# Kernel tuning notes

Measured on AMD Instinct MI355X. Metric: run time of the kernel, lower is better.

## Reference

```python
import jax, jax.numpy as jnp
import numpy as np

B, CHUNKS, INS, H, H2, OS = 128, 2, 512, 256, 512, 64


def setup_inputs() -> dict:
    key = jax.random.key(0)
    ks = jax.random.split(key, 12)
    s = 1.0 / np.sqrt(H)  # torch default LSTM/Linear init scale
    x = jax.random.normal(ks[0], (B, CHUNKS, INS), dtype=jnp.float32)
    w_ih = jax.random.uniform(ks[1], (4 * H, 1), jnp.float32, -s, s)
    w_hh = jax.random.uniform(ks[2], (4 * H, H), jnp.float32, -s, s)
    b_ih = jax.random.uniform(ks[3], (4 * H,), jnp.float32, -s, s)
    b_hh = jax.random.uniform(ks[4], (4 * H,), jnp.float32, -s, s)
    s1 = 1.0 / np.sqrt(INS * H)
    w1 = jax.random.uniform(ks[5], (H, INS * H), jnp.float32, -s1, s1)
    b1 = jax.random.uniform(ks[6], (H,), jnp.float32, -s1, s1)
    w2 = jax.random.uniform(ks[7], (H2, H), jnp.float32, -s, s)
    b2 = jax.random.uniform(ks[8], (H2,), jnp.float32, -s, s)
    s2 = 1.0 / np.sqrt(H2)
    w3 = jax.random.uniform(ks[9], (OS, H2), jnp.float32, -s2, s2)
    b3 = jax.random.uniform(ks[10], (OS,), jnp.float32, -s2, s2)
    return {"x": x, "w_ih": w_ih, "w_hh": w_hh, "b_ih": b_ih, "b_hh": b_hh,
            "w1": w1, "b1": b1, "w2": w2, "b2": b2, "w3": w3, "b3": b3}


def _lstm_scan(xseq, w_ih, w_hh, b_ih, b_hh):
    # xseq: (B, T) scalar-input sequence; returns per-step hidden states (T, B, H)
    wi = w_ih[:, 0]            # (4H,) since input_size == 1
    b = b_ih + b_hh            # (4H,)
    h0 = jnp.zeros((xseq.shape[0], w_hh.shape[1]), xseq.dtype)
    c0 = jnp.zeros_like(h0)

    def step(carry, xt):
        h, c = carry
        gates = xt[:, None] * wi + h @ w_hh.T + b        # (B, 4H)
        i_g, f_g, g_g, o_g = jnp.split(gates, 4, axis=1)  # torch order i,f,g,o
        i_g = jax.nn.sigmoid(i_g)
        f_g = jax.nn.sigmoid(f_g)
        g_g = jnp.tanh(g_g)
        o_g = jax.nn.sigmoid(o_g)
        c = f_g * c + i_g * g_g
        h = o_g * jnp.tanh(c)
        return (h, c), h

    _, hs = jax.lax.scan(step, (h0, c0), xseq.T)  # hs: (T, B, H)
    return hs


def reference(x, w_ih, w_hh, b_ih, b_hh, w1, b1, w2, b2, w3, b3):
    Bx, chunks, ins = x.shape
    # torch: x.view(B, ins, chunks) reinterprets memory, then loops over chunks
    # feeding (B, ins, 1) into the LSTM with hidden carried across chunks ->
    # one long sequence of length chunks*ins, concatenated chunk by chunk.
    x_r = x.reshape(Bx, ins, chunks)
    xseq = jnp.moveaxis(x_r, 2, 1).reshape(Bx, chunks * ins)  # (B, T)
    hs = _lstm_scan(xseq, w_ih, w_hh, b_ih, b_hh)             # (T, B, H)
    # `out` is the LSTM output of the LAST chunk only: (B, ins, H)
    out = jnp.transpose(hs[-ins:], (1, 0, 2)).reshape(Bx, ins * hs.shape[2])
    res1 = jax.nn.relu(out @ w1.T + b1)   # (B, H)
    res2 = res1 @ w2.T + b2               # (B, H2)
    res3 = res2 @ w3.T + b3               # (B, OS)  -- sel=True branch
    return res3
```

## Files before the change

### kernel.cpp

```cpp
#include <hip/hip_runtime.h>
#include <hip/hip_fp16.h>

#define B_    128
#define T_    1024
#define H_    256
#define NTH   512
#define NREG  96
#define NQR   (NREG / 4)
#define NQL   8

typedef _Float16 half2_t __attribute__((ext_vector_type(2)));

__device__ __forceinline__ float fdot2(unsigned int w, unsigned int h, float acc) {
    return __builtin_amdgcn_fdot2(__builtin_bit_cast(half2_t, w),
                                  __builtin_bit_cast(half2_t, h), acc, false);
}
__device__ __forceinline__ unsigned int packf16(float a, float b) {
    half2_t h;
    h.x = (_Float16)a;
    h.y = (_Float16)b;
    return __builtin_bit_cast(unsigned int, h);
}

__global__ __launch_bounds__(NTH, 1) void lstm_k(
    const float* __restrict__ x, const float* __restrict__ w_ih,
    const float* __restrict__ w_hh, const float* __restrict__ b_ih,
    const float* __restrict__ b_hh, unsigned int* __restrict__ hT_p) {
    extern __shared__ unsigned char smem[];
    uint4*        w_lds4 = (uint4*)smem;
    unsigned int* h_u32  = (unsigned int*)(smem + 131072);
    __half*       h_half = (__half*)(smem + 131072);
    float*        gates  = (float*)(smem + 131072 + 512);
    float*        xseq   = (float*)(smem + 131072 + 512 + 4096);

    const int tid = threadIdx.x;
    const int b   = blockIdx.x;
    const int r0  = tid, r1 = tid + NTH;
    const int u   = tid & 255;
    const int g0  = tid >> 8;

    const float bs0 = b_ih[r0] + b_hh[r0], wi0 = w_ih[r0];
    const float bs1 = b_ih[r1] + b_hh[r1], wi1 = w_ih[r1];

    for (int t = tid; t < T_; t += NTH)
        xseq[t] = x[b * T_ + ((t & 511) << 1) + (t >> 9)];

    unsigned int wr0[NREG], wr1[NREG];
#pragma unroll
    for (int p = 0; p < NREG; p += 2) {
        float4 a = *(const float4*)&w_hh[r0 * H_ + 2 * p];
        wr0[p] = packf16(a.x, a.y); wr0[p + 1] = packf16(a.z, a.w);
        float4 c = *(const float4*)&w_hh[r1 * H_ + 2 * p];
        wr1[p] = packf16(c.x, c.y); wr1[p + 1] = packf16(c.z, c.w);
    }
    for (int idx = tid; idx < 1024 * NQL; idx += NTH) {
        int g = idx >> 10, row = idx & 1023;
        const float4* src = (const float4*)&w_hh[row * H_ + 2 * (NREG + 4 * g)];
        float4 a = src[0], c = src[1];
        uint4 pk;
        pk.x = packf16(a.x, a.y); pk.y = packf16(a.z, a.w);
        pk.z = packf16(c.x, c.y); pk.w = packf16(c.z, c.w);
        w_lds4[idx] = pk;
    }
    if (tid < 128) h_u32[tid] = 0u;
    float c_state = 0.f;
    __syncthreads();

    const uint4* h4 = (const uint4*)h_u32;

    for (int t = 0; t < T_; ++t) {
        const float xt = xseq[t];
        float a00 = fmaf(xt, wi0, bs0), a01 = 0.f;
        float a10 = fmaf(xt, wi1, bs1), a11 = 0.f;
#pragma unroll
        for (int q = 0; q < NQR; ++q) {
            uint4 hp = h4[q];
            a00 = fdot2(wr0[4 * q + 0], hp.x, a00);
            a01 = fdot2(wr0[4 * q + 1], hp.y, a01);
            a10 = fdot2(wr1[4 * q + 0], hp.x, a10);
            a11 = fdot2(wr1[4 * q + 1], hp.y, a11);
            a00 = fdot2(wr0[4 * q + 2], hp.z, a00);
            a01 = fdot2(wr0[4 * q + 3], hp.w, a01);
            a10 = fdot2(wr1[4 * q + 2], hp.z, a10);
            a11 = fdot2(wr1[4 * q + 3], hp.w, a11);
        }
#pragma unroll
        for (int q = 0; q < NQL; ++q) {
            uint4 hp = h4[NQR + q];
            uint4 w0 = w_lds4[(q << 10) | r0];
            uint4 w1 = w_lds4[(q << 10) | r1];
            a00 = fdot2(w0.x, hp.x, a00);
            a01 = fdot2(w0.y, hp.y, a01);
            a10 = fdot2(w1.x, hp.x, a10);
            a11 = fdot2(w1.y, hp.y, a11);
            a00 = fdot2(w0.z, hp.z, a00);
            a01 = fdot2(w0.w, hp.w, a01);
            a10 = fdot2(w1.z, hp.z, a10);
            a11 = fdot2(w1.w, hp.w, a11);
        }
        gates[g0 * 256 + u]       = a00 + a01;
        gates[(g0 + 2) * 256 + u] = a10 + a11;
        __syncthreads();
        if (tid < H_) {
            float gi = gates[tid], gf = gates[256 + tid];
            float gg = gates[512 + tid], go = gates[768 + tid];
            float i_ = __builtin_amdgcn_rcpf(1.f + __expf(-gi));
            float f_ = __builtin_amdgcn_rcpf(1.f + __expf(-gf));
            float g_ = 1.f - 2.f * __builtin_amdgcn_rcpf(__expf(2.f * gg) + 1.f);
            float o_ = __builtin_amdgcn_rcpf(1.f + __expf(-go));
            c_state = f_ * c_state + i_ * g_;
            float h = o_ * (1.f - 2.f * __builtin_amdgcn_rcpf(__expf(2.f * c_state) + 1.f));
            h_half[tid] = __float2half(h);
        }
        __syncthreads();
        if (t >= 512 && tid < 128)
            hT_p[(size_t)(((t - 512) << 7) + tid) * B_ + b] = h_u32[tid];
    }
}

#define WST 260
__global__ __launch_bounds__(256, 2) void gemm1_k(
    const unsigned int* __restrict__ hT_p, const float* __restrict__ w1,
    float* __restrict__ part) {
    __shared__ unsigned int w_stage[16 * WST];

    const int tid = threadIdx.x;
    const int m0  = blockIdx.x * 16;
    const int ks  = blockIdx.y;
    const int bl  = tid & 127;
    const int mg  = tid >> 7;
    const int srow = tid >> 4, slane = tid & 15;

    float acc[8];
#pragma unroll
    for (int j = 0; j < 8; ++j) acc[j] = 0.f;

    const int kbase = ks * 2048;
    for (int s = 0; s < 8; ++s) {
        const int k0 = kbase + s * 256;
        __syncthreads();
        const float* wrow = &w1[(size_t)(m0 + srow) * 131072 + 2 * k0];
#pragma unroll
        for (int i = 0; i < 8; ++i) {
            const int f = slane + 16 * i;
            float4 v = *(const float4*)&wrow[4 * f];
            w_stage[srow * WST + 2 * f]     = packf16(v.x, v.y);
            w_stage[srow * WST + 2 * f + 1] = packf16(v.z, v.w);
        }
        __syncthreads();
#pragma unroll 4
        for (int kg = 0; kg < 64; ++kg) {
            const int kp = 4 * kg;
            unsigned int h0 = hT_p[(size_t)(k0 + kp) * B_ + bl];
            unsigned int h1 = hT_p[(size_t)(k0 + kp + 1) * B_ + bl];
            unsigned int h2 = hT_p[(size_t)(k0 + kp + 2) * B_ + bl];
            unsigned int h3 = hT_p[(size_t)(k0 + kp + 3) * B_ + bl];
#pragma unroll
            for (int j = 0; j < 8; ++j) {
                uint4 w = *(const uint4*)&w_stage[(mg * 8 + j) * WST + kp];
                acc[j] = fdot2(w.x, h0, acc[j]);
                acc[j] = fdot2(w.y, h1, acc[j]);
                acc[j] = fdot2(w.z, h2, acc[j]);
                acc[j] = fdot2(w.w, h3, acc[j]);
            }
        }
    }
#pragma unroll
    for (int j = 0; j < 8; ++j)
        part[(size_t)(ks * 256 + m0 + mg * 8 + j) * B_ + bl] = acc[j];
}

__global__ __launch_bounds__(128, 8) void reduce_k(
    const float* __restrict__ part, const float* __restrict__ b1,
    float* __restrict__ res1T) {
    const int m = blockIdx.x, bl = threadIdx.x;
    float s = b1[m];
#pragma unroll 8
    for (int kc = 0; kc < 32; ++kc)
        s += part[(size_t)(kc * 256 + m) * B_ + bl];
    res1T[m * B_ + bl] = fmaxf(s, 0.f);
}

__global__ __launch_bounds__(512, 2) void head_k(
    const float* __restrict__ res1T, const float* __restrict__ w2,
    const float* __restrict__ b2, const float* __restrict__ w3,
    const float* __restrict__ b3, float* __restrict__ out) {
    __shared__ float r1s[256];
    __shared__ float r2s[512];
    const int tid = threadIdx.x;
    const int b   = blockIdx.x;

    if (tid < 256) r1s[tid] = res1T[tid * B_ + b];
    __syncthreads();
    {
        float s = b2[tid];
        const float* wr = &w2[tid * 256];
#pragma unroll 4
        for (int k = 0; k < 256; k += 4) {
            float4 w = *(const float4*)&wr[k];
            s += r1s[k] * w.x + r1s[k + 1] * w.y + r1s[k + 2] * w.z + r1s[k + 3] * w.w;
        }
        r2s[tid] = s;
    }
    __syncthreads();
    if (tid < 64) {
        float s = b3[tid];
        const float* wr = &w3[tid * 512];
#pragma unroll 4
        for (int k = 0; k < 512; k += 4) {
            float4 w = *(const float4*)&wr[k];
            s += r2s[k] * w.x + r2s[k + 1] * w.y + r2s[k + 2] * w.z + r2s[k + 3] * w.w;
        }
        out[b * 64 + tid] = s;
    }
}

extern "C" void kernel_launch(void* const* d_in, const int* in_sizes, int n_in,
                              void* d_out, int out_size, void* d_ws, size_t ws_size,
                              hipStream_t stream) {
    (void)in_sizes; (void)n_in; (void)out_size; (void)ws_size;
    const float* x    = (const float*)d_in[0];
    const float* w_ih = (const float*)d_in[1];
    const float* w_hh = (const float*)d_in[2];
    const float* b_ih = (const float*)d_in[3];
    const float* b_hh = (const float*)d_in[4];
    const float* w1   = (const float*)d_in[5];
    const float* b1   = (const float*)d_in[6];
    const float* w2   = (const float*)d_in[7];
    const float* b2   = (const float*)d_in[8];
    const float* w3   = (const float*)d_in[9];
    const float* b3   = (const float*)d_in[10];
    float* out = (float*)d_out;

    unsigned int* hT_p  = (unsigned int*)d_ws;
    float*        part  = (float*)((char*)d_ws + ((size_t)32 << 20));
    float*        res1T = (float*)((char*)d_ws + ((size_t)40 << 20));

    const size_t smem1 = 131072 + 512 + 4096 + 4096;
    (void)hipFuncSetAttribute((const void*)lstm_k,
                              hipFuncAttributeMaxDynamicSharedMemorySize, (int)smem1);

    hipLaunchKernelGGL(lstm_k, dim3(B_), dim3(NTH), smem1, stream,
                       x, w_ih, w_hh, b_ih, b_hh, hT_p);
    hipLaunchKernelGGL(gemm1_k, dim3(16, 32), dim3(256), 0, stream, hT_p, w1, part);
    hipLaunchKernelGGL(reduce_k, dim3(256), dim3(128), 0, stream, part, b1, res1T);
    hipLaunchKernelGGL(head_k, dim3(B_), dim3(512), 0, stream,
                       res1T, w2, b2, w3, b3, out);
}
```

Baseline: 1.866 ms.

## Compute all four LSTM gates per thread and double-buffer the hidden state

The LSTM kernel now uses 256 threads, each computing the i, f, g and o gate rows for one hidden unit, instead of 512 threads computing two rows each. Because each thread holds all four gate pre-activations, the LDS gates array and its round trip disappear, and the cell update runs on every thread. The hidden state is double-buffered, so each time step needs only one barrier instead of two. In exchange each thread keeps about 448 packed-fp16 weight registers, which risks spills, and each SIMD has only one wave to hide latency.

```diff
diff --git a/kernel.cpp b/kernel.cpp
--- a/kernel.cpp
+++ b/kernel.cpp
@@ -3,11 +3,10 @@
 
 #define B_    128
 #define T_    1024
-#define H_    256
-#define NTH   512
-#define NREG  96
-#define NQR   (NREG / 4)
-#define NQL   8
+#define NTH   256
+#define NREG  112
+#define NQR   28
+#define NQL   4
 
 typedef _Float16 half2_t __attribute__((ext_vector_type(2)));
 
@@ -22,99 +21,102 @@
     return __builtin_bit_cast(unsigned int, h);
 }
 
-__global__ __launch_bounds__(NTH, 1) void lstm_k(
-    const float* __restrict__ x, const float* __restrict__ w_ih,
-    const float* __restrict__ w_hh, const float* __restrict__ b_ih,
-    const float* __restrict__ b_hh, unsigned int* __restrict__ hT_p) {
+__global__ __attribute__((amdgpu_flat_work_group_size(NTH, NTH),
+                          amdgpu_waves_per_eu(1, 1)))
+void lstm_k(const float* __restrict__ x, const float* __restrict__ w_ih,
+            const float* __restrict__ w_hh, const float* __restrict__ b_ih,
+            const float* __restrict__ b_hh, unsigned int* __restrict__ hT_p) {
     extern __shared__ unsigned char smem[];
     uint4*        w_lds4 = (uint4*)smem;
-    unsigned int* h_u32  = (unsigned int*)(smem + 131072);
-    __half*       h_half = (__half*)(smem + 131072);
-    float*        gates  = (float*)(smem + 131072 + 512);
-    float*        xseq   = (float*)(smem + 131072 + 512 + 4096);
-
-    const int tid = threadIdx.x;
-    const int b   = blockIdx.x;
-    const int r0  = tid, r1 = tid + NTH;
-    const int u   = tid & 255;
-    const int g0  = tid >> 8;
-
-    const float bs0 = b_ih[r0] + b_hh[r0], wi0 = w_ih[r0];
-    const float bs1 = b_ih[r1] + b_hh[r1], wi1 = w_ih[r1];
-
-    for (int t = tid; t < T_; t += NTH)
+    unsigned int* hbuf   = (unsigned int*)(smem + 65536);
+    float*        xseq   = (float*)(smem + 65536 + 1024);
+
+    const int u = threadIdx.x;
+    const int b = blockIdx.x;
+
+    float bs[4], wi[4];
+#pragma unroll
+    for (int g = 0; g < 4; ++g) {
+        const int r = g * 256 + u;
+        bs[g] = b_ih[r] + b_hh[r];
+        wi[g] = w_ih[r];
+    }
+
+    for (int t = u; t < T_; t += NTH)
         xseq[t] = x[b * T_ + ((t & 511) << 1) + (t >> 9)];
 
-    unsigned int wr0[NREG], wr1[NREG];
-#pragma unroll
-    for (int p = 0; p < NREG; p += 2) {
-        float4 a = *(const float4*)&w_hh[r0 * H_ + 2 * p];
-        wr0[p] = packf16(a.x, a.y); wr0[p + 1] = packf16(a.z, a.w);
-        float4 c = *(const float4*)&w_hh[r1 * H_ + 2 * p];
-        wr1[p] = packf16(c.x, c.y); wr1[p + 1] = packf16(c.z, c.w);
-    }
-    for (int idx = tid; idx < 1024 * NQL; idx += NTH) {
-        int g = idx >> 10, row = idx & 1023;
-        const float4* src = (const float4*)&w_hh[row * H_ + 2 * (NREG + 4 * g)];
-        float4 a = src[0], c = src[1];
-        uint4 pk;
-        pk.x = packf16(a.x, a.y); pk.y = packf16(a.z, a.w);
-        pk.z = packf16(c.x, c.y); pk.w = packf16(c.z, c.w);
-        w_lds4[idx] = pk;
-    }
-    if (tid < 128) h_u32[tid] = 0u;
+    unsigned int wr[4][NREG];
+#pragma unroll
+    for (int g = 0; g < 4; ++g) {
+        const float* row = &w_hh[(size_t)(g * 256 + u) * 256];
+#pragma unroll
+        for (int p = 0; p < NREG; p += 2) {
+            float4 a4 = *(const float4*)&row[2 * p];
+            wr[g][p]     = packf16(a4.x, a4.y);
+            wr[g][p + 1] = packf16(a4.z, a4.w);
+        }
+    }
+#pragma unroll
+    for (int g = 0; g < 4; ++g) {
+#pragma unroll
+        for (int q = 0; q < NQL; ++q) {
+            const float* src = &w_hh[(size_t)(g * 256 + u) * 256 + 2 * NREG + 8 * q];
+            float4 a4 = ((const float4*)src)[0];
+            float4 c4 = ((const float4*)src)[1];
+            uint4 pk;
+            pk.x = packf16(a4.x, a4.y); pk.y = packf16(a4.z, a4.w);
+            pk.z = packf16(c4.x, c4.y); pk.w = packf16(c4.z, c4.w);
+            w_lds4[(g * NQL + q) * 256 + u] = pk;
+        }
+    }
+    if (u < 128) { hbuf[u] = 0u; hbuf[128 + u] = 0u; }
     float c_state = 0.f;
     __syncthreads();
 
-    const uint4* h4 = (const uint4*)h_u32;
-
     for (int t = 0; t < T_; ++t) {
-        const float xt = xseq[t];
-        float a00 = fmaf(xt, wi0, bs0), a01 = 0.f;
-        float a10 = fmaf(xt, wi1, bs1), a11 = 0.f;
+        const uint4* h4 = (const uint4*)&hbuf[(t & 1) * 128];
+        const float  xt = xseq[t];
+        float a0[4], a1[4];
+#pragma unroll
+        for (int g = 0; g < 4; ++g) {
+            a0[g] = fmaf(xt, wi[g], bs[g]);
+            a1[g] = 0.f;
+        }
 #pragma unroll
         for (int q = 0; q < NQR; ++q) {
             uint4 hp = h4[q];
-            a00 = fdot2(wr0[4 * q + 0], hp.x, a00);
-            a01 = fdot2(wr0[4 * q + 1], hp.y, a01);
-            a10 = fdot2(wr1[4 * q + 0], hp.x, a10);
-            a11 = fdot2(wr1[4 * q + 1], hp.y, a11);
-            a00 = fdot2(wr0[4 * q + 2], hp.z, a00);
-            a01 = fdot2(wr0[4 * q + 3], hp.w, a01);
-            a10 = fdot2(wr1[4 * q + 2], hp.z, a10);
-            a11 = fdot2(wr1[4 * q + 3], hp.w, a11);
+#pragma unroll
+            for (int g = 0; g < 4; ++g) {
+                a0[g] = fdot2(wr[g][4 * q + 0], hp.x, a0[g]);
+                a1[g] = fdot2(wr[g][4 * q + 1], hp.y, a1[g]);
+                a0[g] = fdot2(wr[g][4 * q + 2], hp.z, a0[g]);
+                a1[g] = fdot2(wr[g][4 * q + 3], hp.w, a1[g]);
+            }
         }
 #pragma unroll
         for (int q = 0; q < NQL; ++q) {
             uint4 hp = h4[NQR + q];
-            uint4 w0 = w_lds4[(q << 10) | r0];
-            uint4 w1 = w_lds4[(q << 10) | r1];
-            a00 = fdot2(w0.x, hp.x, a00);
-            a01 = fdot2(w0.y, hp.y, a01);
-            a10 = fdot2(w1.x, hp.x, a10);
-            a11 = fdot2(w1.y, hp.y, a11);
-            a00 = fdot2(w0.z, hp.z, a00);
-            a01 = fdot2(w0.w, hp.w, a01);
-            a10 = fdot2(w1.z, hp.z, a10);
-            a11 = fdot2(w1.w, hp.w, a11);
-        }
-        gates[g0 * 256 + u]       = a00 + a01;
-        gates[(g0 + 2) * 256 + u] = a10 + a11;
+#pragma unroll
+            for (int g = 0; g < 4; ++g) {
+                uint4 w = w_lds4[(g * NQL + q) * 256 + u];
+                a0[g] = fdot2(w.x, hp.x, a0[g]);
+                a1[g] = fdot2(w.y, hp.y, a1[g]);
+                a0[g] = fdot2(w.z, hp.z, a0[g]);
+                a1[g] = fdot2(w.w, hp.w, a1[g]);
+            }
+        }
+        const float gi = a0[0] + a1[0], gf = a0[1] + a1[1];
+        const float gg = a0[2] + a1[2], go = a0[3] + a1[3];
+        const float i_ = __builtin_amdgcn_rcpf(1.f + __expf(-gi));
+        const float f_ = __builtin_amdgcn_rcpf(1.f + __expf(-gf));
+        const float g_ = 1.f - 2.f * __builtin_amdgcn_rcpf(__expf(2.f * gg) + 1.f);
+        const float o_ = __builtin_amdgcn_rcpf(1.f + __expf(-go));
+        c_state = f_ * c_state + i_ * g_;
+        const float h = o_ * (1.f - 2.f * __builtin_amdgcn_rcpf(__expf(2.f * c_state) + 1.f));
+        ((__half*)&hbuf[((t + 1) & 1) * 128])[u] = __float2half(h);
         __syncthreads();
-        if (tid < H_) {
-            float gi = gates[tid], gf = gates[256 + tid];
-            float gg = gates[512 + tid], go = gates[768 + tid];
-            float i_ = __builtin_amdgcn_rcpf(1.f + __expf(-gi));
-            float f_ = __builtin_amdgcn_rcpf(1.f + __expf(-gf));
-            float g_ = 1.f - 2.f * __builtin_amdgcn_rcpf(__expf(2.f * gg) + 1.f);
-            float o_ = __builtin_amdgcn_rcpf(1.f + __expf(-go));
-            c_state = f_ * c_state + i_ * g_;
-            float h = o_ * (1.f - 2.f * __builtin_amdgcn_rcpf(__expf(2.f * c_state) + 1.f));
-            h_half[tid] = __float2half(h);
-        }
-        __syncthreads();
-        if (t >= 512 && tid < 128)
-            hT_p[(size_t)(((t - 512) << 7) + tid) * B_ + b] = h_u32[tid];
+        if (t >= 512 && u < 128)
+            hT_p[(size_t)(((t - 512) << 7) + u) * B_ + b] = hbuf[((t + 1) & 1) * 128 + u];
     }
 }
 
@@ -236,7 +238,7 @@
     float*        part  = (float*)((char*)d_ws + ((size_t)32 << 20));
     float*        res1T = (float*)((char*)d_ws + ((size_t)40 << 20));
 
-    const size_t smem1 = 131072 + 512 + 4096 + 4096;
+    const size_t smem1 = 65536 + 1024 + 4096;
     (void)hipFuncSetAttribute((const void*)lstm_k,
                               hipFuncAttributeMaxDynamicSharedMemorySize, (int)smem1);
 
```

Result: slower. 2.999 ms (+60.7%).
